# Kernel optimization log

Measured on AMD Instinct MI355X. Metric: run time of the kernel, lower is better.

The kernel has to match this reference:

```python
import jax, jax.numpy as jnp
import numpy as np

T, B, D, H = 2048, 32, 256, 256


def setup_inputs() -> dict:
    key = jax.random.key(0)
    ks = jax.random.split(key, 7)
    s = 1.0 / np.sqrt(H)
    return {
        "seq_embs": jax.random.normal(ks[0], (T, B, D), dtype=jnp.float32),
        "mask_x": jax.random.randint(ks[1], (T, B), 0, 2, dtype=jnp.int32),
        "hidden": jax.random.normal(ks[2], (B, H), dtype=jnp.float32),
        "w_ih": jax.random.uniform(ks[3], (3 * H, D), jnp.float32, -s, s),
        "w_hh": jax.random.uniform(ks[4], (3 * H, H), jnp.float32, -s, s),
        "b_ih": jax.random.uniform(ks[5], (3 * H,), jnp.float32, -s, s),
        "b_hh": jax.random.uniform(ks[6], (3 * H,), jnp.float32, -s, s),
    }


def reference(seq_embs, mask_x, hidden, w_ih, w_hh, b_ih, b_hh):
    # Precompute all input-side gate projections in one big GEMM: [T, B, 3H]
    gi_all = jnp.einsum("tbd,gd->tbg", seq_embs, w_ih) + b_ih
    mask_f = mask_x.astype(seq_embs.dtype)  # [T, B]

    def step(h, inp):
        gi, m_t = inp  # gi: [B, 3H], m_t: [B]
        gh = h @ w_hh.T + b_hh  # [B, 3H]
        i_r, i_z, i_n = jnp.split(gi, 3, axis=1)
        h_r, h_z, h_n = jnp.split(gh, 3, axis=1)
        r = jax.nn.sigmoid(i_r + h_r)
        z = jax.nn.sigmoid(i_z + h_z)
        n = jnp.tanh(i_n + r * h_n)
        h_t = (1.0 - z) * n + z * h  # GRUCell candidate hidden
        m = m_t[:, None]  # [B, 1]
        h_new = h_t * m + h * (1.0 - m)  # mask-gated state update
        return h_new, h_t * m  # output per step is masked candidate

    h_final, outputs = jax.lax.scan(step, hidden, (gi_all, mask_f))
    return outputs, h_final
```

## Files before the change

kernel.cpp:

```cpp
#include <hip/hip_runtime.h>
#include <hip/hip_bf16.h>

#define TT 2048
#define BB 32
#define DD 256
#define HH 256
#define GG 768

typedef _Float16 half2_t __attribute__((ext_vector_type(2)));
typedef _Float16 f16x8 __attribute__((ext_vector_type(8)));
typedef float    f32x4 __attribute__((ext_vector_type(4)));

__device__ inline float fdot2(unsigned int w, unsigned int h, float acc) {
#if __has_builtin(__builtin_amdgcn_fdot2)
    return __builtin_amdgcn_fdot2(__builtin_bit_cast(half2_t, w),
                                  __builtin_bit_cast(half2_t, h), acc, false);
#else
    half2_t a = __builtin_bit_cast(half2_t, w);
    half2_t b = __builtin_bit_cast(half2_t, h);
    return acc + (float)a.x * (float)b.x + (float)a.y * (float)b.y;
#endif
}

__device__ inline float ldgi(const float* p) { return *p; }
__device__ inline float ldgi(const __hip_bfloat16* p) { return __bfloat162float(*p); }
__device__ inline void stgi(float* p, float v) { *p = v; }
__device__ inline void stgi(__hip_bfloat16* p, float v) { *p = __float2bfloat16(v); }

__global__ __launch_bounds__(256)
void pack_w(const float* __restrict__ w, unsigned int* __restrict__ wpk) {
    int i = blockIdx.x * 256 + threadIdx.x;
    int q = i / GG;
    int j = i - q * GG;
    float a = w[(size_t)j * DD + 2 * q];
    float b = w[(size_t)j * DD + 2 * q + 1];
    half2_t h = {(_Float16)a, (_Float16)b};
    wpk[i] = __builtin_bit_cast(unsigned int, h);
}

template <typename GiT>
__global__ __launch_bounds__(256)
void gemm_gi_mfma(const float* __restrict__ A,
                  const float* __restrict__ W,
                  const float* __restrict__ bias,
                  GiT* __restrict__ C)
{
    __shared__ __align__(16) _Float16 Asl[128][40];
    __shared__ __align__(16) _Float16 Bsl[128][40];

    const int tid = threadIdx.x;
    const int wv  = tid >> 6;
    const int l   = tid & 63;
    const int wm  = (wv & 1) * 64;
    const int wn  = (wv >> 1) * 64;
    const size_t bm = (size_t)blockIdx.y * 128;
    const int    bn = blockIdx.x * 128;

    const int lr = tid >> 3;
    const int lc = (tid & 7) * 4;

    f32x4 acc[4][4] = {};

    for (int kt = 0; kt < 256; kt += 32) {
#pragma unroll
        for (int rr = 0; rr < 128; rr += 32) {
            float4 av = *(const float4*)&A[(bm + lr + rr) * DD + kt + lc];
            half2_t p0 = {(_Float16)av.x, (_Float16)av.y};
            half2_t p1 = {(_Float16)av.z, (_Float16)av.w};
            uint2 pk = {__builtin_bit_cast(unsigned int, p0),
                        __builtin_bit_cast(unsigned int, p1)};
            *(uint2*)&Asl[lr + rr][lc] = pk;
        }
#pragma unroll
        for (int rr = 0; rr < 128; rr += 32) {
            float4 bv = *(const float4*)&W[(size_t)(bn + lr + rr) * DD + kt + lc];
            half2_t p0 = {(_Float16)bv.x, (_Float16)bv.y};
            half2_t p1 = {(_Float16)bv.z, (_Float16)bv.w};
            uint2 pk = {__builtin_bit_cast(unsigned int, p0),
                        __builtin_bit_cast(unsigned int, p1)};
            *(uint2*)&Bsl[lr + rr][lc] = pk;
        }
        __syncthreads();

        f16x8 af[4], bf[4];
#pragma unroll
        for (int i = 0; i < 4; ++i) {
            af[i] = *(const f16x8*)&Asl[wm + i * 16 + (l & 15)][(l >> 4) * 8];
            bf[i] = *(const f16x8*)&Bsl[wn + i * 16 + (l & 15)][(l >> 4) * 8];
        }
#pragma unroll
        for (int mi = 0; mi < 4; ++mi)
#pragma unroll
            for (int ni = 0; ni < 4; ++ni)
                acc[mi][ni] = __builtin_amdgcn_mfma_f32_16x16x32_f16(
                    af[mi], bf[ni], acc[mi][ni], 0, 0, 0);
        __syncthreads();
    }

    const int crow = (l >> 4) * 4;
    const int ccol = l & 15;
#pragma unroll
    for (int ni = 0; ni < 4; ++ni) {
        int n = bn + wn + ni * 16 + ccol;
        float bs = bias[n];
#pragma unroll
        for (int mi = 0; mi < 4; ++mi) {
#pragma unroll
            for (int q = 0; q < 4; ++q) {
                size_t m = bm + wm + mi * 16 + crow + q;
                stgi(&C[m * GG + n], acc[mi][ni][q] + bs);
            }
        }
    }
}

template <typename GiT>
__global__ void
__attribute__((amdgpu_flat_work_group_size(768, 768), amdgpu_waves_per_eu(3, 3)))
gru_scan(const GiT* __restrict__ gi,
         const int* __restrict__ mask,
         const float* __restrict__ h0,
         const unsigned int* __restrict__ wpk,
         const float* __restrict__ b_hh,
         float* __restrict__ out,
         float* __restrict__ hfin)
{
    const int b = blockIdx.x;
    const int j = threadIdx.x;
    __shared__ __align__(16) _Float16 hhalf[HH];
    __shared__ float gh_lds[GG];
    __shared__ int mlds[TT];

    unsigned int w[128];
#pragma unroll
    for (int q = 0; q < 128; ++q)
        w[q] = wpk[q * GG + j];
#pragma unroll
    for (int q = 0; q < 128; ++q)
        asm volatile("" : "+v"(w[q]));

    for (int t = j; t < TT; t += GG)
        mlds[t] = mask[t * BB + b];

    float h_r = 0.f;
    if (j < HH) {
        h_r = h0[b * HH + j];
        hhalf[j] = (_Float16)h_r;
    }
    const float bhh = b_hh[j];
    __syncthreads();

    const uint4* hu4 = (const uint4*)hhalf;

    for (int t = 0; t < TT; ++t) {
        if (mlds[t]) {
            float ir = 0.f, iz = 0.f, inn = 0.f;
            if (j < HH) {
                const GiT* gtb = gi + ((size_t)t * BB + b) * GG;
                ir  = ldgi(gtb + j);
                iz  = ldgi(gtb + j + HH);
                inn = ldgi(gtb + j + 2 * HH);
            }

            float a0 = bhh, a1 = 0.f, a2 = 0.f, a3 = 0.f;
#pragma unroll
            for (int q4 = 0; q4 < 32; ++q4) {
                uint4 hv = hu4[q4];
                a0 = fdot2(w[4 * q4 + 0], hv.x, a0);
                a1 = fdot2(w[4 * q4 + 1], hv.y, a1);
                a2 = fdot2(w[4 * q4 + 2], hv.z, a2);
                a3 = fdot2(w[4 * q4 + 3], hv.w, a3);
            }
            gh_lds[j] = (a0 + a1) + (a2 + a3);
            __syncthreads();

            if (j < HH) {
                float hr = gh_lds[j];
                float hz = gh_lds[j + HH];
                float hn = gh_lds[j + 2 * HH];
                float r = 1.f / (1.f + __expf(-(ir + hr)));
                float z = 1.f / (1.f + __expf(-(iz + hz)));
                float e = __expf(2.f * (inn + r * hn));
                float n = 1.f - 2.f / (e + 1.f);
                float ht = (1.f - z) * n + z * h_r;
                out[((size_t)t * BB + b) * HH + j] = ht;
                h_r = ht;
                hhalf[j] = (_Float16)ht;
            }
            __syncthreads();
        } else {
            if (j < HH)
                out[((size_t)t * BB + b) * HH + j] = 0.f;
        }
    }
    if (j < HH) hfin[b * HH + j] = h_r;
}

extern "C" void kernel_launch(void* const* d_in, const int* in_sizes, int n_in,
                              void* d_out, int out_size, void* d_ws, size_t ws_size,
                              hipStream_t stream) {
    const float* seq  = (const float*)d_in[0];
    const int*   mask = (const int*)  d_in[1];
    const float* h0   = (const float*)d_in[2];
    const float* w_ih = (const float*)d_in[3];
    const float* w_hh = (const float*)d_in[4];
    const float* b_ih = (const float*)d_in[5];
    const float* b_hh = (const float*)d_in[6];

    float* out  = (float*)d_out;
    float* hfin = out + (size_t)TT * BB * HH;

    const size_t wpk_elems = (size_t)128 * GG;
    unsigned int* wpk = (unsigned int*)d_ws;
    const size_t gi_elems = (size_t)TT * BB * GG;
    const size_t need_f32 = wpk_elems * 4 + gi_elems * 4;

    pack_w<<<(128 * GG) / 256, 256, 0, stream>>>(w_hh, wpk);

    dim3 ggrid(GG / 128, (TT * BB) / 128);
    if (ws_size >= need_f32) {
        float* gip = (float*)d_ws + wpk_elems;
        gemm_gi_mfma<float><<<ggrid, 256, 0, stream>>>(seq, w_ih, b_ih, gip);
        gru_scan<float><<<BB, GG, 0, stream>>>(gip, mask, h0, wpk, b_hh, out, hfin);
    } else {
        __hip_bfloat16* gip = (__hip_bfloat16*)((float*)d_ws + wpk_elems);
        gemm_gi_mfma<__hip_bfloat16><<<ggrid, 256, 0, stream>>>(seq, w_ih, b_ih, gip);
        gru_scan<__hip_bfloat16><<<BB, GG, 0, stream>>>(gip, mask, h0, wpk, b_hh, out, hfin);
    }
}
```

Measured before the change: 1.572 ms.

## Compute all three gates per thread in GRU scan, dropping gate exchange via LDS

The recurrent scan now uses 256 threads per batch element. Each thread holds the r, z and n weight rows in registers and computes its three gate dot products directly, instead of 768 threads each computing one gate row and exchanging results through shared memory. The weight packing layout is changed to uint4 groups per gate so these loads are vectorized. This removes the gh shared-memory round trip and lets every thread do the elementwise update. The cost is much higher register pressure (single wave per SIMD) and less latency hiding.

```diff
diff --git a/kernel.cpp b/kernel.cpp
--- a/kernel.cpp
+++ b/kernel.cpp
@@ -28,14 +28,20 @@
 __device__ inline void stgi(__hip_bfloat16* p, float v) { *p = __float2bfloat16(v); }
 
 __global__ __launch_bounds__(256)
-void pack_w(const float* __restrict__ w, unsigned int* __restrict__ wpk) {
+void pack_w(const float* __restrict__ w, unsigned int* __restrict__ wf) {
     int i = blockIdx.x * 256 + threadIdx.x;
-    int q = i / GG;
-    int j = i - q * GG;
-    float a = w[(size_t)j * DD + 2 * q];
-    float b = w[(size_t)j * DD + 2 * q + 1];
+    int c = i & 3;
+    int e = i >> 2;
+    int t = e & 255;
+    int gg4 = e >> 8;
+    int g4 = gg4 & 31;
+    int gate = gg4 >> 5;
+    int n = gate * 256 + t;
+    int k = g4 * 8 + 2 * c;
+    float a = w[(size_t)n * DD + k];
+    float b = w[(size_t)n * DD + k + 1];
     half2_t h = {(_Float16)a, (_Float16)b};
-    wpk[i] = __builtin_bit_cast(unsigned int, h);
+    wf[i] = __builtin_bit_cast(unsigned int, h);
 }
 
 template <typename GiT>
@@ -116,84 +122,86 @@
 
 template <typename GiT>
 __global__ void
-__attribute__((amdgpu_flat_work_group_size(768, 768), amdgpu_waves_per_eu(3, 3)))
+__attribute__((amdgpu_flat_work_group_size(256, 256), amdgpu_waves_per_eu(1, 1)))
 gru_scan(const GiT* __restrict__ gi,
          const int* __restrict__ mask,
          const float* __restrict__ h0,
-         const unsigned int* __restrict__ wpk,
+         const uint4* __restrict__ wq,
          const float* __restrict__ b_hh,
          float* __restrict__ out,
          float* __restrict__ hfin)
 {
     const int b = blockIdx.x;
-    const int j = threadIdx.x;
+    const int t = threadIdx.x;
     __shared__ __align__(16) _Float16 hhalf[HH];
-    __shared__ float gh_lds[GG];
     __shared__ int mlds[TT];
 
-    unsigned int w[128];
-#pragma unroll
-    for (int q = 0; q < 128; ++q)
-        w[q] = wpk[q * GG + j];
-#pragma unroll
-    for (int q = 0; q < 128; ++q)
-        asm volatile("" : "+v"(w[q]));
-
-    for (int t = j; t < TT; t += GG)
-        mlds[t] = mask[t * BB + b];
-
-    float h_r = 0.f;
-    if (j < HH) {
-        h_r = h0[b * HH + j];
-        hhalf[j] = (_Float16)h_r;
-    }
-    const float bhh = b_hh[j];
+    uint4 wr[32], wz[32], wn_[32];
+#pragma unroll
+    for (int g4 = 0; g4 < 32; ++g4) wr[g4]  = wq[(0 * 32 + g4) * 256 + t];
+#pragma unroll
+    for (int g4 = 0; g4 < 32; ++g4) wz[g4]  = wq[(1 * 32 + g4) * 256 + t];
+#pragma unroll
+    for (int g4 = 0; g4 < 32; ++g4) wn_[g4] = wq[(2 * 32 + g4) * 256 + t];
+
+    for (int i = t; i < TT; i += 256)
+        mlds[i] = mask[i * BB + b];
+
+    float h_r = h0[b * HH + t];
+    hhalf[t] = (_Float16)h_r;
+    const float bhr = b_hh[t];
+    const float bhz = b_hh[t + HH];
+    const float bhn = b_hh[t + 2 * HH];
     __syncthreads();
 
     const uint4* hu4 = (const uint4*)hhalf;
 
-    for (int t = 0; t < TT; ++t) {
-        if (mlds[t]) {
-            float ir = 0.f, iz = 0.f, inn = 0.f;
-            if (j < HH) {
-                const GiT* gtb = gi + ((size_t)t * BB + b) * GG;
-                ir  = ldgi(gtb + j);
-                iz  = ldgi(gtb + j + HH);
-                inn = ldgi(gtb + j + 2 * HH);
+    for (int ts = 0; ts < TT; ++ts) {
+        if (mlds[ts]) {
+            const GiT* gtb = gi + ((size_t)ts * BB + b) * GG;
+            float ir  = ldgi(gtb + t);
+            float iz  = ldgi(gtb + t + HH);
+            float inn = ldgi(gtb + t + 2 * HH);
+
+            float r0 = bhr, r1 = 0.f, r2 = 0.f, r3 = 0.f;
+            float z0 = bhz, z1 = 0.f, z2 = 0.f, z3 = 0.f;
+            float n0 = bhn, n1 = 0.f, n2 = 0.f, n3 = 0.f;
+#pragma unroll
+            for (int g4 = 0; g4 < 32; ++g4) {
+                uint4 hv = hu4[g4];
+                r0 = fdot2(wr[g4].x, hv.x, r0);
+                r1 = fdot2(wr[g4].y, hv.y, r1);
+                r2 = fdot2(wr[g4].z, hv.z, r2);
+                r3 = fdot2(wr[g4].w, hv.w, r3);
+                z0 = fdot2(wz[g4].x, hv.x, z0);
+                z1 = fdot2(wz[g4].y, hv.y, z1);
+                z2 = fdot2(wz[g4].z, hv.z, z2);
+                z3 = fdot2(wz[g4].w, hv.w, z3);
+                n0 = fdot2(wn_[g4].x, hv.x, n0);
+                n1 = fdot2(wn_[g4].y, hv.y, n1);
+                n2 = fdot2(wn_[g4].z, hv.z, n2);
+                n3 = fdot2(wn_[g4].w, hv.w, n3);
             }
-
-            float a0 = bhh, a1 = 0.f, a2 = 0.f, a3 = 0.f;
-#pragma unroll
-            for (int q4 = 0; q4 < 32; ++q4) {
-                uint4 hv = hu4[q4];
-                a0 = fdot2(w[4 * q4 + 0], hv.x, a0);
-                a1 = fdot2(w[4 * q4 + 1], hv.y, a1);
-                a2 = fdot2(w[4 * q4 + 2], hv.z, a2);
-                a3 = fdot2(w[4 * q4 + 3], hv.w, a3);
-            }
-            gh_lds[j] = (a0 + a1) + (a2 + a3);
+            float hr = (r0 + r1) + (r2 + r3);
+            float hz = (z0 + z1) + (z2 + z3);
+            float hn = (n0 + n1) + (n2 + n3);
+
+            float r = 1.f / (1.f + __expf(-(ir + hr)));
+            float z = 1.f / (1.f + __expf(-(iz + hz)));
+            float e = __expf(2.f * (inn + r * hn));
+            float n = 1.f - 2.f / (e + 1.f);
+            float ht = (1.f - z) * n + z * h_r;
+
             __syncthreads();
-
-            if (j < HH) {
-                float hr = gh_lds[j];
-                float hz = gh_lds[j + HH];
-                float hn = gh_lds[j + 2 * HH];
-                float r = 1.f / (1.f + __expf(-(ir + hr)));
-                float z = 1.f / (1.f + __expf(-(iz + hz)));
-                float e = __expf(2.f * (inn + r * hn));
-                float n = 1.f - 2.f / (e + 1.f);
-                float ht = (1.f - z) * n + z * h_r;
-                out[((size_t)t * BB + b) * HH + j] = ht;
-                h_r = ht;
-                hhalf[j] = (_Float16)ht;
-            }
+            out[((size_t)ts * BB + b) * HH + t] = ht;
+            h_r = ht;
+            hhalf[t] = (_Float16)ht;
             __syncthreads();
         } else {
-            if (j < HH)
-                out[((size_t)t * BB + b) * HH + j] = 0.f;
-        }
-    }
-    if (j < HH) hfin[b * HH + j] = h_r;
+            out[((size_t)ts * BB + b) * HH + t] = 0.f;
+        }
+    }
+    hfin[b * HH + t] = h_r;
 }
 
 extern "C" void kernel_launch(void* const* d_in, const int* in_sizes, int n_in,
@@ -210,21 +218,24 @@
     float* out  = (float*)d_out;
     float* hfin = out + (size_t)TT * BB * HH;
 
-    const size_t wpk_elems = (size_t)128 * GG;
-    unsigned int* wpk = (unsigned int*)d_ws;
+    const size_t w_u32 = (size_t)128 * GG;
+    unsigned int* wf = (unsigned int*)d_ws;
     const size_t gi_elems = (size_t)TT * BB * GG;
-    const size_t need_f32 = wpk_elems * 4 + gi_elems * 4;
-
-    pack_w<<<(128 * GG) / 256, 256, 0, stream>>>(w_hh, wpk);
+    const size_t need_f32 = w_u32 * 4 + gi_elems * 4;
+
+    pack_w<<<(int)(w_u32 / 256), 256, 0, stream>>>(w_hh, wf);
 
     dim3 ggrid(GG / 128, (TT * BB) / 128);
     if (ws_size >= need_f32) {
-        float* gip = (float*)d_ws + wpk_elems;
+        float* gip = (float*)d_ws + w_u32;
         gemm_gi_mfma<float><<<ggrid, 256, 0, stream>>>(seq, w_ih, b_ih, gip);
-        gru_scan<float><<<BB, GG, 0, stream>>>(gip, mask, h0, wpk, b_hh, out, hfin);
+        gru_scan<float><<<BB, 256, 0, stream>>>(gip, mask, h0, (const uint4*)wf,
+                                                b_hh, out, hfin);
     } else {
-        __hip_bfloat16* gip = (__hip_bfloat16*)((float*)d_ws + wpk_elems);
+        __hip_bfloat16* gip = (__hip_bfloat16*)((float*)d_ws + w_u32);
         gemm_gi_mfma<__hip_bfloat16><<<ggrid, 256, 0, stream>>>(seq, w_ih, b_ih, gip);
-        gru_scan<__hip_bfloat16><<<BB, GG, 0, stream>>>(gip, mask, h0, wpk, b_hh, out, hfin);
-    }
-}
+        gru_scan<__hip_bfloat16><<<BB, 256, 0, stream>>>(gip, mask, h0,
+                                                         (const uint4*)wf,
+                                                         b_hh, out, hfin);
+    }
+}
```

After: 2.976 ms. 1.89x slower.

## Remap GRU scan to 512 threads with split n-gate rows and AGPR weights

Applied to the files above, without the earlier changes.

The recurrent matvec now runs on 512 threads instead of 768. Each thread owns one full r/z row (128 packed weights), and pairs of threads split each n-gate row in halves (64 packed weights each). The halves are combined with a lane shuffle before the LDS write. Weights are repacked for uint4 loads, pinned to accumulator registers, and the recurrent bias is added in the gate stage. The aim is to cut per-step barrier and wave overhead on the latency-bound serial scan, at the cost of a longer per-thread dot product and register pressure from 192 weight registers.

```diff
diff --git a/kernel.cpp b/kernel.cpp
--- a/kernel.cpp
+++ b/kernel.cpp
@@ -28,14 +28,23 @@
 __device__ inline void stgi(__hip_bfloat16* p, float v) { *p = __float2bfloat16(v); }
 
 __global__ __launch_bounds__(256)
-void pack_w(const float* __restrict__ w, unsigned int* __restrict__ wpk) {
+void pack_w(const float* __restrict__ w, unsigned int* __restrict__ wf) {
     int i = blockIdx.x * 256 + threadIdx.x;
-    int q = i / GG;
-    int j = i - q * GG;
-    float a = w[(size_t)j * DD + 2 * q];
-    float b = w[(size_t)j * DD + 2 * q + 1];
+    int col, k;
+    if (i < 65536) {
+        int comp = i & 3, t = (i >> 2) & 511, q4 = i >> 11;
+        col = t;
+        k = 8 * q4 + 2 * comp;
+    } else {
+        int i2 = i - 65536;
+        int comp = i2 & 3, t = (i2 >> 2) & 511, p4 = i2 >> 11;
+        col = 512 + (t >> 1);
+        k = (t & 1) * 128 + 8 * p4 + 2 * comp;
+    }
+    float a = w[(size_t)col * DD + k];
+    float b = w[(size_t)col * DD + k + 1];
     half2_t h = {(_Float16)a, (_Float16)b};
-    wpk[i] = __builtin_bit_cast(unsigned int, h);
+    wf[i] = __builtin_bit_cast(unsigned int, h);
 }
 
 template <typename GiT>
@@ -116,7 +125,7 @@
 
 template <typename GiT>
 __global__ void
-__attribute__((amdgpu_flat_work_group_size(768, 768), amdgpu_waves_per_eu(3, 3)))
+__attribute__((amdgpu_flat_work_group_size(512, 512), amdgpu_waves_per_eu(2, 2)))
 gru_scan(const GiT* __restrict__ gi,
          const int* __restrict__ mask,
          const float* __restrict__ h0,
@@ -126,74 +135,111 @@
          float* __restrict__ hfin)
 {
     const int b = blockIdx.x;
-    const int j = threadIdx.x;
+    const int t = threadIdx.x;
     __shared__ __align__(16) _Float16 hhalf[HH];
     __shared__ float gh_lds[GG];
     __shared__ int mlds[TT];
 
-    unsigned int w[128];
+    unsigned int wA[128];
+    unsigned int wB[64];
+    {
+        const uint4* wp = (const uint4*)wpk;
+#pragma unroll
+        for (int q4 = 0; q4 < 32; ++q4) {
+            uint4 v = wp[q4 * 512 + t];
+            wA[4 * q4 + 0] = v.x;
+            wA[4 * q4 + 1] = v.y;
+            wA[4 * q4 + 2] = v.z;
+            wA[4 * q4 + 3] = v.w;
+        }
+        const uint4* wpB = wp + 32 * 512;
+#pragma unroll
+        for (int p4 = 0; p4 < 16; ++p4) {
+            uint4 v = wpB[p4 * 512 + t];
+            wB[4 * p4 + 0] = v.x;
+            wB[4 * p4 + 1] = v.y;
+            wB[4 * p4 + 2] = v.z;
+            wB[4 * p4 + 3] = v.w;
+        }
+    }
 #pragma unroll
     for (int q = 0; q < 128; ++q)
-        w[q] = wpk[q * GG + j];
-#pragma unroll
-    for (int q = 0; q < 128; ++q)
-        asm volatile("" : "+v"(w[q]));
-
-    for (int t = j; t < TT; t += GG)
-        mlds[t] = mask[t * BB + b];
-
-    float h_r = 0.f;
-    if (j < HH) {
-        h_r = h0[b * HH + j];
-        hhalf[j] = (_Float16)h_r;
-    }
-    const float bhh = b_hh[j];
+        asm volatile("" : "+a"(wA[q]));
+#pragma unroll
+    for (int q = 0; q < 64; ++q)
+        asm volatile("" : "+a"(wB[q]));
+
+    for (int i = t; i < TT; i += 512)
+        mlds[i] = mask[i * BB + b];
+
+    float h_r = 0.f, bh0 = 0.f, bh1 = 0.f, bh2 = 0.f;
+    if (t < HH) {
+        h_r = h0[b * HH + t];
+        hhalf[t] = (_Float16)h_r;
+        bh0 = b_hh[t];
+        bh1 = b_hh[t + HH];
+        bh2 = b_hh[t + 2 * HH];
+    }
     __syncthreads();
 
     const uint4* hu4 = (const uint4*)hhalf;
-
-    for (int t = 0; t < TT; ++t) {
-        if (mlds[t]) {
+    const uint4* hB  = (const uint4*)(hhalf + (t & 1) * 128);
+
+    for (int ts = 0; ts < TT; ++ts) {
+        if (mlds[ts]) {
             float ir = 0.f, iz = 0.f, inn = 0.f;
-            if (j < HH) {
-                const GiT* gtb = gi + ((size_t)t * BB + b) * GG;
-                ir  = ldgi(gtb + j);
-                iz  = ldgi(gtb + j + HH);
-                inn = ldgi(gtb + j + 2 * HH);
-            }
-
-            float a0 = bhh, a1 = 0.f, a2 = 0.f, a3 = 0.f;
+            if (t < HH) {
+                const GiT* gtb = gi + ((size_t)ts * BB + b) * GG;
+                ir  = ldgi(gtb + t);
+                iz  = ldgi(gtb + t + HH);
+                inn = ldgi(gtb + t + 2 * HH);
+            }
+
+            float a0 = 0.f, a1 = 0.f, a2 = 0.f, a3 = 0.f;
 #pragma unroll
             for (int q4 = 0; q4 < 32; ++q4) {
                 uint4 hv = hu4[q4];
-                a0 = fdot2(w[4 * q4 + 0], hv.x, a0);
-                a1 = fdot2(w[4 * q4 + 1], hv.y, a1);
-                a2 = fdot2(w[4 * q4 + 2], hv.z, a2);
-                a3 = fdot2(w[4 * q4 + 3], hv.w, a3);
-            }
-            gh_lds[j] = (a0 + a1) + (a2 + a3);
+                a0 = fdot2(wA[4 * q4 + 0], hv.x, a0);
+                a1 = fdot2(wA[4 * q4 + 1], hv.y, a1);
+                a2 = fdot2(wA[4 * q4 + 2], hv.z, a2);
+                a3 = fdot2(wA[4 * q4 + 3], hv.w, a3);
+            }
+            float c0 = 0.f, c1 = 0.f, c2 = 0.f, c3 = 0.f;
+#pragma unroll
+            for (int p4 = 0; p4 < 16; ++p4) {
+                uint4 hv = hB[p4];
+                c0 = fdot2(wB[4 * p4 + 0], hv.x, c0);
+                c1 = fdot2(wB[4 * p4 + 1], hv.y, c1);
+                c2 = fdot2(wB[4 * p4 + 2], hv.z, c2);
+                c3 = fdot2(wB[4 * p4 + 3], hv.w, c3);
+            }
+            float accB = (c0 + c1) + (c2 + c3);
+            float accBo = __shfl_xor(accB, 1);
+            gh_lds[t] = (a0 + a1) + (a2 + a3);
+            if (!(t & 1))
+                gh_lds[512 + (t >> 1)] = accB + accBo;
             __syncthreads();
 
-            if (j < HH) {
-                float hr = gh_lds[j];
-                float hz = gh_lds[j + HH];
-                float hn = gh_lds[j + 2 * HH];
+            if (t < HH) {
+                float hr = gh_lds[t] + bh0;
+                float hz = gh_lds[t + HH] + bh1;
+                float hn = gh_lds[t + 2 * HH] + bh2;
                 float r = 1.f / (1.f + __expf(-(ir + hr)));
                 float z = 1.f / (1.f + __expf(-(iz + hz)));
                 float e = __expf(2.f * (inn + r * hn));
                 float n = 1.f - 2.f / (e + 1.f);
                 float ht = (1.f - z) * n + z * h_r;
-                out[((size_t)t * BB + b) * HH + j] = ht;
+                out[((size_t)ts * BB + b) * HH + t] = ht;
                 h_r = ht;
-                hhalf[j] = (_Float16)ht;
+                hhalf[t] = (_Float16)ht;
             }
             __syncthreads();
         } else {
-            if (j < HH)
-                out[((size_t)t * BB + b) * HH + j] = 0.f;
-        }
-    }
-    if (j < HH) hfin[b * HH + j] = h_r;
+            if (t < HH)
+                out[((size_t)ts * BB + b) * HH + t] = 0.f;
+        }
+    }
+    if (t < HH) hfin[b * HH + t] = h_r;
 }
 
 extern "C" void kernel_launch(void* const* d_in, const int* in_sizes, int n_in,
@@ -215,16 +261,16 @@
     const size_t gi_elems = (size_t)TT * BB * GG;
     const size_t need_f32 = wpk_elems * 4 + gi_elems * 4;
 
-    pack_w<<<(128 * GG) / 256, 256, 0, stream>>>(w_hh, wpk);
+    pack_w<<<(int)(wpk_elems / 256), 256, 0, stream>>>(w_hh, wpk);
 
     dim3 ggrid(GG / 128, (TT * BB) / 128);
     if (ws_size >= need_f32) {
         float* gip = (float*)d_ws + wpk_elems;
         gemm_gi_mfma<float><<<ggrid, 256, 0, stream>>>(seq, w_ih, b_ih, gip);
-        gru_scan<float><<<BB, GG, 0, stream>>>(gip, mask, h0, wpk, b_hh, out, hfin);
+        gru_scan<float><<<BB, 512, 0, stream>>>(gip, mask, h0, wpk, b_hh, out, hfin);
     } else {
         __hip_bfloat16* gip = (__hip_bfloat16*)((float*)d_ws + wpk_elems);
         gemm_gi_mfma<__hip_bfloat16><<<ggrid, 256, 0, stream>>>(seq, w_ih, b_ih, gip);
-        gru_scan<__hip_bfloat16><<<BB, GG, 0, stream>>>(gip, mask, h0, wpk, b_hh, out, hfin);
-    }
-}
+        gru_scan<__hip_bfloat16><<<BB, 512, 0, stream>>>(gip, mask, h0, wpk, b_hh, out, hfin);
+    }
+}
```

Result: slower. 2.323 ms (+47.8%).
